# Kernel tuning notes

Hardware: AMD Instinct MI355X
Metric: run time of the kernel (lower is better)

The kernel has to match this reference:

```python
import jax, jax.numpy as jnp
import numpy as np

EPS = 1e-5
SLOPE = 0.01  # nn.LeakyReLU default


def _subm_conv(feats, W, nbr):
    # feats: [N_in, Cin]; W: [K, Cin, Cout]; nbr: [K, N_out] with sentinel N_in -> zero
    padded = jnp.concatenate([feats, jnp.zeros((1, feats.shape[1]), feats.dtype)], axis=0)
    g = padded[nbr]  # [K, N_out, Cin] gather (rulebook gather stage)
    return jnp.einsum('knc,kcd->nd', g, W)  # GEMM + scatter-accumulate over offsets


def _lrelu(x):
    return jnp.where(x >= 0, x, SLOPE * x)


def _bn(x, gamma, beta):
    # BatchNorm1d in training mode: batch stats over point dim, biased variance
    m = jnp.mean(x, axis=0)
    v = jnp.mean(jnp.square(x - m), axis=0)
    return (x - m) * jax.lax.rsqrt(v + EPS) * gamma + beta


def setup_inputs() -> dict:
    key = jax.random.key(0)
    ks = jax.random.split(key, 12)
    N_in, N_out, Cin, Cout = 80000, 200000, 128, 64
    inp = {
        'x_feats': jax.random.normal(ks[0], (N_in, Cin), jnp.float32),
        'skip_feats': jax.random.normal(ks[1], (N_out, Cout), jnp.float32),
        'nbr_trans': jax.random.randint(ks[2], (27, N_in), 0, N_in + 1, jnp.int32),
        'nbr_up': jax.random.randint(ks[3], (27, N_out), 0, N_in + 1, jnp.int32),
        'nbr1': jax.random.randint(ks[4], (9, N_out), 0, N_out + 1, jnp.int32),
        'nbr2': jax.random.randint(ks[5], (9, N_out), 0, N_out + 1, jnp.int32),
        'nbr3': jax.random.randint(ks[6], (27, N_out), 0, N_out + 1, jnp.int32),
        'W_trans': jax.random.normal(ks[7], (27, Cin, Cout), jnp.float32) * 0.05,
        'W_up': jax.random.normal(ks[8], (27, Cout, Cout), jnp.float32) * 0.05,
        'W1': jax.random.normal(ks[9], (9, Cout, Cout), jnp.float32) * 0.05,
        'W2': jax.random.normal(ks[10], (9, Cout, Cout), jnp.float32) * 0.05,
        'W3': jax.random.normal(ks[11], (27, Cout, Cout), jnp.float32) * 0.05,
        'gamma_t': jnp.ones((Cout,), jnp.float32), 'beta_t': jnp.zeros((Cout,), jnp.float32),
        'gamma1': jnp.ones((Cout,), jnp.float32), 'beta1': jnp.zeros((Cout,), jnp.float32),
        'gamma2': jnp.ones((Cout,), jnp.float32), 'beta2': jnp.zeros((Cout,), jnp.float32),
        'gamma3': jnp.ones((Cout,), jnp.float32), 'beta3': jnp.zeros((Cout,), jnp.float32),
    }
    return inp


def reference(x_feats, skip_feats, nbr_trans, nbr_up, nbr1, nbr2, nbr3,
              W_trans, W_up, W1, W2, W3,
              gamma_t, beta_t, gamma1, beta1, gamma2, beta2, gamma3, beta3):
    # trans_dilao (SubMConv3d 3x3x3) + LeakyReLU + BN
    h = _subm_conv(x_feats, W_trans, nbr_trans)          # [N_in, Cout]
    h = _bn(_lrelu(h), gamma_t, beta_t)
    # SparseInverseConv3d: gather from coarse points into dense output set
    u = _subm_conv(h, W_up, nbr_up)                      # [N_out, Cout]
    u = u + skip_feats                                   # residual skip add
    # conv1 (1x3x3) + act + bn
    e = _bn(_lrelu(_subm_conv(u, W1, nbr1)), gamma1, beta1)
    # conv2 (3x1x3) + act + bn
    e = _bn(_lrelu(_subm_conv(e, W2, nbr2)), gamma2, beta2)
    # conv3 (3x3x3) + act + bn
    e = _bn(_lrelu(_subm_conv(e, W3, nbr3)), gamma3, beta3)
    return e
```

## Files before the change

### kernel.cpp

```cpp
#include <hip/hip_runtime.h>

#define EPS 1e-5f
#define SLOPE 0.01f

typedef __attribute__((ext_vector_type(8))) short bf16x8;
typedef __attribute__((ext_vector_type(4))) float f32x4;

static __device__ __forceinline__ unsigned short f2bf(float f) {
    unsigned u = __float_as_uint(f);
    u += 0x7fff + ((u >> 16) & 1);
    return (unsigned short)(u >> 16);
}
static __device__ __forceinline__ float bf2f(unsigned short h) {
    return __uint_as_float(((unsigned)h) << 16);
}

static __device__ __forceinline__ void gload16(const unsigned short* g, void* l) {
    __builtin_amdgcn_global_load_lds(
        (const __attribute__((address_space(1))) unsigned int*)g,
        (__attribute__((address_space(3))) unsigned int*)l,
        16, 0, 0);
}

template<int K, int NCH>
__global__ __launch_bounds__(256, 3)
void conv_mfma(const unsigned short* __restrict__ in, int tableN,
               const int* __restrict__ nbr, int Nout,
               const unsigned short* __restrict__ Wt2,
               const float* __restrict__ skip,
               unsigned short* __restrict__ out_bf,
               float* __restrict__ out_f32,
               float* __restrict__ stats, int do_lrelu)
{
    constexpr int Cin = NCH * 64;
    constexpr int KT  = K * NCH;

    __shared__ unsigned short Abuf[2][128 * 64];
    __shared__ int   sIdx[K * 128];
    __shared__ float red[2][64][4];

    const int t    = threadIdx.x;
    const int lane = t & 63;
    const int w    = t >> 6;
    const int q    = lane >> 4;
    const int m    = lane & 15;
    const int row0 = blockIdx.x * 128;
    const int wrow = w * 32;

    const int glr = lane >> 3;
    const int gls = lane & 7;

    for (int e = t; e < K * 128; e += 256) {
        int k = e >> 7, r = e & 127;
        int gr = row0 + r;
        sIdx[e] = (gr < Nout) ? nbr[(size_t)k * Nout + gr] : tableN;
    }
    __syncthreads();

    f32x4 acc[2][4];
#pragma unroll
    for (int rt = 0; rt < 2; ++rt)
#pragma unroll
        for (int ct = 0; ct < 4; ++ct) acc[rt][ct] = (f32x4){0.f, 0.f, 0.f, 0.f};

    auto gather = [&](int kk, int p) {
        const int k  = kk / NCH;
        const int cc = kk % NCH;
        const int* sI = &sIdx[k * 128 + wrow];
#pragma unroll
        for (int j = 0; j < 4; ++j) {
            int src = sI[j * 8 + glr];
            const unsigned short* g =
                in + (size_t)src * Cin + cc * 64 + gls * 8;
            gload16(g, (void*)&Abuf[p][(wrow + j * 8) * 64]);
        }
    };
    auto loadB = [&](int kk, bf16x8 (&bb)[2][4]) {
#pragma unroll
        for (int kc = 0; kc < 2; ++kc)
#pragma unroll
            for (int ct = 0; ct < 4; ++ct)
                bb[kc][ct] = *(const bf16x8*)(
                    Wt2 + (((size_t)(kk * 2 + kc) * 4 + ct) * 64 + lane) * 8);
    };

    bf16x8 bR[2][2][4];
    gather(0, 0);
    loadB(0, bR[0]);
    __syncthreads();

#pragma unroll
    for (int kk = 0; kk < KT; ++kk) {
        const int p = kk & 1;
        if (kk + 1 < KT) {
            gather(kk + 1, p ^ 1);
            loadB(kk + 1, bR[p ^ 1]);
        }
        bf16x8 a[2][2];
#pragma unroll
        for (int kc = 0; kc < 2; ++kc)
#pragma unroll
            for (int rt = 0; rt < 2; ++rt)
                a[kc][rt] = *(const bf16x8*)
                    &Abuf[p][(wrow + rt * 16 + m) * 64 + (kc * 4 + q) * 8];
#pragma unroll
        for (int kc = 0; kc < 2; ++kc)
#pragma unroll
            for (int rt = 0; rt < 2; ++rt)
#pragma unroll
                for (int ct = 0; ct < 4; ++ct)
                    acc[rt][ct] = __builtin_amdgcn_mfma_f32_16x16x32_bf16(
                        a[kc][rt], bR[p][kc][ct], acc[rt][ct], 0, 0, 0);
        __syncthreads();
    }

    float psum[4] = {0.f, 0.f, 0.f, 0.f}, psq[4] = {0.f, 0.f, 0.f, 0.f};
#pragma unroll
    for (int rt = 0; rt < 2; ++rt) {
#pragma unroll
        for (int ct = 0; ct < 4; ++ct) {
            int col = ct * 16 + m;
#pragma unroll
            for (int reg = 0; reg < 4; ++reg) {
                int r = row0 + wrow + rt * 16 + q * 4 + reg;
                if (r < Nout) {
                    float v = acc[rt][ct][reg];
                    if (skip) v += skip[(size_t)r * 64 + col];
                    if (do_lrelu) v = (v >= 0.f) ? v : SLOPE * v;
                    if (out_bf) out_bf[(size_t)r * 64 + col] = f2bf(v);
                    else        out_f32[(size_t)r * 64 + col] = v;
                    psum[ct] += v;
                    psq[ct]  += v * v;
                }
            }
        }
    }

    if (stats) {
#pragma unroll
        for (int ct = 0; ct < 4; ++ct) {
            psum[ct] += __shfl_down(psum[ct], 32);
            psum[ct] += __shfl_down(psum[ct], 16);
            psq[ct]  += __shfl_down(psq[ct], 32);
            psq[ct]  += __shfl_down(psq[ct], 16);
        }
        if (q == 0) {
#pragma unroll
            for (int ct = 0; ct < 4; ++ct) {
                red[0][ct * 16 + m][w] = psum[ct];
                red[1][ct * 16 + m][w] = psq[ct];
            }
        }
        __syncthreads();
        if (t < 64) {
            float s  = red[0][t][0] + red[0][t][1] + red[0][t][2] + red[0][t][3];
            float qq = red[1][t][0] + red[1][t][1] + red[1][t][2] + red[1][t][3];
            atomicAdd(&stats[t], s);
            atomicAdd(&stats[64 + t], qq);
        }
    }
}

__global__ __launch_bounds__(256)
void bn_apply_bf16(unsigned short* __restrict__ buf, size_t total8,
                   const float* __restrict__ stats,
                   const float* __restrict__ gamma,
                   const float* __restrict__ beta, float invN)
{
    __shared__ float sc[64], sh[64];
    int t = threadIdx.x;
    if (t < 64) {
        float mean = stats[t] * invN;
        float var  = stats[64 + t] * invN - mean * mean;
        float s    = gamma[t] * rsqrtf(var + EPS);
        sc[t] = s;
        sh[t] = beta[t] - mean * s;
    }
    __syncthreads();
    for (size_t i = (size_t)blockIdx.x * blockDim.x + t; i < total8;
         i += (size_t)gridDim.x * blockDim.x) {
        int4 v = ((const int4*)buf)[i];
        unsigned short* e = (unsigned short*)&v;
        int c0 = ((int)(i & 7)) << 3;
#pragma unroll
        for (int j = 0; j < 8; ++j)
            e[j] = f2bf(bf2f(e[j]) * sc[c0 + j] + sh[c0 + j]);
        ((int4*)buf)[i] = v;
    }
}

__global__ __launch_bounds__(256)
void bn_apply_f32(float* __restrict__ buf, int N,
                  const float* __restrict__ stats,
                  const float* __restrict__ gamma,
                  const float* __restrict__ beta, float invN)
{
    __shared__ float sc[64], sh[64];
    int t = threadIdx.x;
    if (t < 64) {
        float mean = stats[t] * invN;
        float var  = stats[64 + t] * invN - mean * mean;
        float s    = gamma[t] * rsqrtf(var + EPS);
        sc[t] = s;
        sh[t] = beta[t] - mean * s;
    }
    __syncthreads();
    size_t total4 = (size_t)N * 16;
    for (size_t i = (size_t)blockIdx.x * blockDim.x + t; i < total4;
         i += (size_t)gridDim.x * blockDim.x) {
        float4 v = ((const float4*)buf)[i];
        int c0 = ((int)(i & 15)) << 2;
        v.x = v.x * sc[c0]     + sh[c0];
        v.y = v.y * sc[c0 + 1] + sh[c0 + 1];
        v.z = v.z * sc[c0 + 2] + sh[c0 + 2];
        v.w = v.w * sc[c0 + 3] + sh[c0 + 3];
        ((float4*)buf)[i] = v;
    }
}

__global__ __launch_bounds__(256)
void cvt_bf16(const float* __restrict__ in, unsigned short* __restrict__ out,
              size_t n4)
{
    for (size_t i = (size_t)blockIdx.x * blockDim.x + threadIdx.x; i < n4;
         i += (size_t)gridDim.x * blockDim.x) {
        float4 v = ((const float4*)in)[i];
        ushort4 o;
        o.x = f2bf(v.x); o.y = f2bf(v.y); o.z = f2bf(v.z); o.w = f2bf(v.w);
        ((ushort4*)out)[i] = o;
    }
}

__global__ __launch_bounds__(256)
void zero_sentinels(unsigned short* xb, int Nin128,
                    unsigned short* tb, int Nin64,
                    unsigned short* ub, unsigned short* ab, unsigned short* vb,
                    int Nout64)
{
    int t = threadIdx.x;
    if (t < 128) xb[(size_t)Nin128 + t] = 0;
    if (t < 64) {
        tb[(size_t)Nin64 + t] = 0;
        ub[(size_t)Nout64 + t] = 0;
        ab[(size_t)Nout64 + t] = 0;
        vb[(size_t)Nout64 + t] = 0;
    }
}

static __device__ __forceinline__ void wt2_one(int e, const float* __restrict__ W,
                                               unsigned short* __restrict__ Wt2,
                                               int NCH)
{
    int j  = e & 7;
    int l  = (e >> 3) & 63;
    int ct = (e >> 9) & 3;
    int kc = (e >> 11) & 1;
    int kk = e >> 12;
    int qq = l >> 4, mm = l & 15;
    int k  = kk / NCH, cc = kk % NCH;
    int Cin = NCH * 64;
    int c  = cc * 64 + kc * 32 + qq * 8 + j;
    int d  = ct * 16 + mm;
    Wt2[e] = f2bf(W[((size_t)k * Cin + c) * 64 + d]);
}

__global__ __launch_bounds__(256)
void wt_cvt_all(const float* __restrict__ W_trans, const float* __restrict__ W_up,
                const float* __restrict__ W1, const float* __restrict__ W2,
                const float* __restrict__ W3,
                unsigned short* __restrict__ wt_t, unsigned short* __restrict__ wt_u,
                unsigned short* __restrict__ wt1, unsigned short* __restrict__ wt2,
                unsigned short* __restrict__ wt3)
{
    const int S0 = 27 * 128 * 64;
    const int S1 = 27 * 64 * 64;
    const int S2 = 9 * 64 * 64;
    const int S3 = 9 * 64 * 64;
    const int S4 = 27 * 64 * 64;
    int e = blockIdx.x * blockDim.x + threadIdx.x;
    if (e < S0) { wt2_one(e, W_trans, wt_t, 2); return; }
    e -= S0;
    if (e < S1) { wt2_one(e, W_up, wt_u, 1); return; }
    e -= S1;
    if (e < S2) { wt2_one(e, W1, wt1, 1); return; }
    e -= S2;
    if (e < S3) { wt2_one(e, W2, wt2, 1); return; }
    e -= S3;
    if (e < S4) { wt2_one(e, W3, wt3, 1); }
}

extern "C" void kernel_launch(void* const* d_in, const int* in_sizes, int n_in,
                              void* d_out, int out_size, void* d_ws, size_t ws_size,
                              hipStream_t stream) {
    const float* x_feats   = (const float*)d_in[0];
    const float* skip      = (const float*)d_in[1];
    const int*   nbr_trans = (const int*)d_in[2];
    const int*   nbr_up    = (const int*)d_in[3];
    const int*   nbr1      = (const int*)d_in[4];
    const int*   nbr2      = (const int*)d_in[5];
    const int*   nbr3      = (const int*)d_in[6];
    const float* W_trans   = (const float*)d_in[7];
    const float* W_up      = (const float*)d_in[8];
    const float* W1        = (const float*)d_in[9];
    const float* W2        = (const float*)d_in[10];
    const float* W3        = (const float*)d_in[11];
    const float* gamma_t   = (const float*)d_in[12];
    const float* beta_t    = (const float*)d_in[13];
    const float* gamma1    = (const float*)d_in[14];
    const float* beta1     = (const float*)d_in[15];
    const float* gamma2    = (const float*)d_in[16];
    const float* beta2     = (const float*)d_in[17];
    const float* gamma3    = (const float*)d_in[18];
    const float* beta3     = (const float*)d_in[19];

    const int Nin  = in_sizes[0] / 128;
    const int Nout = in_sizes[1] / 64;

    size_t off = 0;
    auto alloc = [&](size_t bytes) {
        void* p = (char*)d_ws + off;
        off = (off + bytes + 255) & ~(size_t)255;
        return p;
    };
    unsigned short* xb   = (unsigned short*)alloc(((size_t)Nin + 1) * 128 * 2);
    unsigned short* tb   = (unsigned short*)alloc(((size_t)Nin + 1) * 64 * 2);
    unsigned short* ub   = (unsigned short*)alloc(((size_t)Nout + 1) * 64 * 2);
    unsigned short* ab   = (unsigned short*)alloc(((size_t)Nout + 1) * 64 * 2);
    unsigned short* vb   = (unsigned short*)alloc(((size_t)Nout + 1) * 64 * 2);
    unsigned short* wt_t = (unsigned short*)alloc((size_t)27 * 128 * 64 * 2);
    unsigned short* wt_u = (unsigned short*)alloc((size_t)27 * 64 * 64 * 2);
    unsigned short* wt1  = (unsigned short*)alloc((size_t)9 * 64 * 64 * 2);
    unsigned short* wt2  = (unsigned short*)alloc((size_t)9 * 64 * 64 * 2);
    unsigned short* wt3  = (unsigned short*)alloc((size_t)27 * 64 * 64 * 2);
    float* stats = (float*)alloc(512 * sizeof(float));
    float* out   = (float*)d_out;

    hipMemsetAsync(stats, 0, 512 * sizeof(float), stream);

    dim3 blk(256);
    const float invNin  = 1.f / (float)Nin;
    const float invNout = 1.f / (float)Nout;

    wt_cvt_all<<<2016, blk, 0, stream>>>(W_trans, W_up, W1, W2, W3,
                                         wt_t, wt_u, wt1, wt2, wt3);
    cvt_bf16<<<2048, blk, 0, stream>>>(x_feats, xb, (size_t)Nin * 32);
    zero_sentinels<<<1, blk, 0, stream>>>(xb, Nin * 128, tb, Nin * 64,
                                          ub, ab, vb, Nout * 64);

    const int gIn  = (Nin  + 127) / 128;
    const int gOut = (Nout + 127) / 128;

    conv_mfma<27, 2><<<gIn, blk, 0, stream>>>(xb, Nin, nbr_trans, Nin,
                                              wt_t, nullptr, tb, nullptr, stats + 0, 1);
    bn_apply_bf16<<<1024, blk, 0, stream>>>(tb, (size_t)Nin * 8, stats + 0,
                                            gamma_t, beta_t, invNin);
    conv_mfma<27, 1><<<gOut, blk, 0, stream>>>(tb, Nin, nbr_up, Nout,
                                               wt_u, skip, ub, nullptr, nullptr, 0);
    conv_mfma<9, 1><<<gOut, blk, 0, stream>>>(ub, Nout, nbr1, Nout,
                                              wt1, nullptr, ab, nullptr, stats + 128, 1);
    bn_apply_bf16<<<2048, blk, 0, stream>>>(ab, (size_t)Nout * 8, stats + 128,
                                            gamma1, beta1, invNout);
    conv_mfma<9, 1><<<gOut, blk, 0, stream>>>(ab, Nout, nbr2, Nout,
                                              wt2, nullptr, vb, nullptr, stats + 256, 1);
    bn_apply_bf16<<<2048, blk, 0, stream>>>(vb, (size_t)Nout * 8, stats + 256,
                                            gamma2, beta2, invNout);
    conv_mfma<27, 1><<<gOut, blk, 0, stream>>>(vb, Nout, nbr3, Nout,
                                               wt3, nullptr, nullptr, out, stats + 384, 1);
    bn_apply_f32<<<2048, blk, 0, stream>>>(out, Nout, stats + 384,
                                           gamma3, beta3, invNout);
}
```

Measured before the change: 724.1 us.

## Gather A rows directly into registers instead of staging through LDS

Replaces the LDS-staged gather (global_load_lds into a double-buffered shared tile, then ds_read per MFMA operand) with direct per-lane global loads of neighbor rows into registers, double-buffered in VGPRs with index prefetch two steps ahead. This removes the shared A buffer and the per-iteration __syncthreads, which also lowers LDS usage. In exchange it uses more registers and issues 16-byte loads per lane in the MFMA operand layout, so coalescing and occupancy may suffer.

```diff
diff --git a/kernel.cpp b/kernel.cpp
--- a/kernel.cpp
+++ b/kernel.cpp
@@ -13,13 +13,6 @@
 }
 static __device__ __forceinline__ float bf2f(unsigned short h) {
     return __uint_as_float(((unsigned)h) << 16);
-}
-
-static __device__ __forceinline__ void gload16(const unsigned short* g, void* l) {
-    __builtin_amdgcn_global_load_lds(
-        (const __attribute__((address_space(1))) unsigned int*)g,
-        (__attribute__((address_space(3))) unsigned int*)l,
-        16, 0, 0);
 }
 
 template<int K, int NCH>
@@ -35,7 +28,6 @@
     constexpr int Cin = NCH * 64;
     constexpr int KT  = K * NCH;
 
-    __shared__ unsigned short Abuf[2][128 * 64];
     __shared__ int   sIdx[K * 128];
     __shared__ float red[2][64][4];
 
@@ -47,9 +39,6 @@
     const int row0 = blockIdx.x * 128;
     const int wrow = w * 32;
 
-    const int glr = lane >> 3;
-    const int gls = lane & 7;
-
     for (int e = t; e < K * 128; e += 256) {
         int k = e >> 7, r = e & 127;
         int gr = row0 + r;
@@ -63,46 +52,46 @@
 #pragma unroll
         for (int ct = 0; ct < 4; ++ct) acc[rt][ct] = (f32x4){0.f, 0.f, 0.f, 0.f};
 
-    auto gather = [&](int kk, int p) {
-        const int k  = kk / NCH;
-        const int cc = kk % NCH;
-        const int* sI = &sIdx[k * 128 + wrow];
-#pragma unroll
-        for (int j = 0; j < 4; ++j) {
-            int src = sI[j * 8 + glr];
-            const unsigned short* g =
-                in + (size_t)src * Cin + cc * 64 + gls * 8;
-            gload16(g, (void*)&Abuf[p][(wrow + j * 8) * 64]);
-        }
+    bf16x8 aR[2][2][2];
+    bf16x8 bR[2][2][4];
+    int    id[2][2];
+
+    auto loadIdx = [&](int kk, int buf) {
+        int k = kk / NCH;
+        id[buf][0] = sIdx[k * 128 + wrow + m];
+        id[buf][1] = sIdx[k * 128 + wrow + 16 + m];
     };
-    auto loadB = [&](int kk, bf16x8 (&bb)[2][4]) {
+    auto loadA = [&](int kk, int buf) {
+        int cc = kk % NCH;
+        const unsigned short* g0 = in + (size_t)id[buf][0] * Cin + cc * 64 + q * 8;
+        const unsigned short* g1 = in + (size_t)id[buf][1] * Cin + cc * 64 + q * 8;
+        aR[buf][0][0] = *(const bf16x8*)g0;
+        aR[buf][1][0] = *(const bf16x8*)(g0 + 32);
+        aR[buf][0][1] = *(const bf16x8*)g1;
+        aR[buf][1][1] = *(const bf16x8*)(g1 + 32);
+    };
+    auto loadB = [&](int kk, int buf) {
 #pragma unroll
         for (int kc = 0; kc < 2; ++kc)
 #pragma unroll
             for (int ct = 0; ct < 4; ++ct)
-                bb[kc][ct] = *(const bf16x8*)(
+                bR[buf][kc][ct] = *(const bf16x8*)(
                     Wt2 + (((size_t)(kk * 2 + kc) * 4 + ct) * 64 + lane) * 8);
     };
 
-    bf16x8 bR[2][2][4];
-    gather(0, 0);
-    loadB(0, bR[0]);
-    __syncthreads();
+    loadIdx(0, 0);
+    loadA(0, 0);
+    loadB(0, 0);
+    if (KT > 1) loadIdx(1, 1);
 
 #pragma unroll
     for (int kk = 0; kk < KT; ++kk) {
         const int p = kk & 1;
         if (kk + 1 < KT) {
-            gather(kk + 1, p ^ 1);
-            loadB(kk + 1, bR[p ^ 1]);
-        }
-        bf16x8 a[2][2];
-#pragma unroll
-        for (int kc = 0; kc < 2; ++kc)
-#pragma unroll
-            for (int rt = 0; rt < 2; ++rt)
-                a[kc][rt] = *(const bf16x8*)
-                    &Abuf[p][(wrow + rt * 16 + m) * 64 + (kc * 4 + q) * 8];
+            loadA(kk + 1, p ^ 1);
+            loadB(kk + 1, p ^ 1);
+        }
+        if (kk + 2 < KT) loadIdx(kk + 2, p);
 #pragma unroll
         for (int kc = 0; kc < 2; ++kc)
 #pragma unroll
@@ -110,8 +99,7 @@
 #pragma unroll
                 for (int ct = 0; ct < 4; ++ct)
                     acc[rt][ct] = __builtin_amdgcn_mfma_f32_16x16x32_bf16(
-                        a[kc][rt], bR[p][kc][ct], acc[rt][ct], 0, 0, 0);
-        __syncthreads();
+                        aR[p][kc][rt], bR[p][kc][ct], acc[rt][ct], 0, 0, 0);
     }
 
     float psum[4] = {0.f, 0.f, 0.f, 0.f}, psq[4] = {0.f, 0.f, 0.f, 0.f};
```

New measurement: 825.3 us. 14.0% more time.
